# Performance work log

Hardware: AMD Instinct MI355X
Metric: run time of the kernel (lower is better)

## Reference

```python
import jax, jax.numpy as jnp
import numpy as np

NUM_HEADS = 8
NUM_LEVELS = 4
NUM_POINTS = 8
EMBED = 256
SPATIAL_SHAPES = ((92, 160), (46, 80), (23, 40), (12, 20))


def _bilinear_sample(vl, gx, gy, H, W):
    # vl: [N, d, H*W]; gx, gy: [N, Q, P], grid coords in [-1, 1]
    # matches F.grid_sample(mode='bilinear', padding_mode='zeros', align_corners=False)
    x = (gx + 1.0) * (W * 0.5) - 0.5
    y = (gy + 1.0) * (H * 0.5) - 0.5
    x0 = jnp.floor(x)
    y0 = jnp.floor(y)
    wx = x - x0
    wy = y - y0
    x0i = x0.astype(jnp.int32)
    y0i = y0.astype(jnp.int32)
    N, Q, P = gx.shape
    d = vl.shape[1]

    def gather(xi, yi):
        valid = ((xi >= 0) & (xi < W) & (yi >= 0) & (yi < H)).astype(vl.dtype)
        idx = jnp.clip(yi, 0, H - 1) * W + jnp.clip(xi, 0, W - 1)  # [N, Q, P]
        flat = jnp.broadcast_to(idx.reshape(N, 1, Q * P), (N, d, Q * P))
        got = jnp.take_along_axis(vl, flat, axis=2).reshape(N, d, Q, P)
        return got * valid[:, None]

    return (gather(x0i, y0i) * ((1 - wx) * (1 - wy))[:, None]
            + gather(x0i + 1, y0i) * (wx * (1 - wy))[:, None]
            + gather(x0i, y0i + 1) * ((1 - wx) * wy)[:, None]
            + gather(x0i + 1, y0i + 1) * (wx * wy)[:, None])


def _forward(query, value, reference_points, spatial_shapes,
             W_off, b_off, W_attn, b_attn, W_val, b_val, W_out, b_out):
    shapes = np.asarray(spatial_shapes)  # static per-level (H, W)
    bs, Q, C = query.shape
    H, Lv, P = NUM_HEADS, NUM_LEVELS, NUM_POINTS
    d = C // H
    # value projection, split into heads: [bs*H, d, Ltot]
    v = value @ W_val + b_val
    v = v.reshape(bs, -1, H, d).transpose(0, 2, 3, 1).reshape(bs * H, d, -1)
    # sampling offsets [bs, Q, H, Lv, P, 2]
    off = (query @ W_off + b_off).reshape(bs, Q, H, Lv, P, 2)
    # attention weights, softmax over Lv*P
    aw = jax.nn.softmax((query @ W_attn + b_attn).reshape(bs, Q, H, Lv * P), axis=-1)
    aw = aw.reshape(bs, Q, H, Lv, P).transpose(0, 2, 1, 3, 4).reshape(bs * H, Q, Lv, P)
    # normalize offsets by level (W, H)
    norm = jnp.asarray([[w_, h_] for h_, w_ in shapes], dtype=query.dtype)  # [Lv, 2]
    loc = reference_points[:, :, None, :, None, :] + off / norm[None, None, None, :, None, :]
    grids = (2.0 * loc - 1.0).transpose(0, 2, 1, 3, 4, 5).reshape(bs * H, Q, Lv, P, 2)
    out = jnp.zeros((bs * H, d, Q), dtype=query.dtype)
    start = 0
    for lvl in range(Lv):
        H_l, W_l = int(shapes[lvl, 0]), int(shapes[lvl, 1])
        vl = v[:, :, start:start + H_l * W_l]
        g = grids[:, :, lvl]  # [bs*H, Q, P, 2]
        s = _bilinear_sample(vl, g[..., 0], g[..., 1], H_l, W_l)  # [bs*H, d, Q, P]
        out = out + jnp.einsum('ndqp,nqp->ndq', s, aw[:, :, lvl])
        start += H_l * W_l
    out = out.reshape(bs, H, d, Q).transpose(0, 3, 1, 2).reshape(bs, Q, C)
    return out @ W_out + b_out


def setup_inputs() -> dict:
    key = jax.random.key(0)
    ks = jax.random.split(key, 9)
    bs, Q = 6, 4096  # 6 cameras x (64x64 BEV queries)
    Ltot = sum(h * w for h, w in SPATIAL_SHAPES)  # 19560
    HLP2 = NUM_HEADS * NUM_LEVELS * NUM_POINTS * 2  # 512
    HLP = NUM_HEADS * NUM_LEVELS * NUM_POINTS  # 256
    s = 0.02
    return {
        "query": jax.random.normal(ks[0], (bs, Q, EMBED), jnp.float32),
        "value": jax.random.normal(ks[1], (bs, Ltot, EMBED), jnp.float32),
        "reference_points": jax.random.uniform(ks[2], (bs, Q, NUM_LEVELS, 2), jnp.float32),
        "spatial_shapes": jnp.asarray(SPATIAL_SHAPES, jnp.int32),
        "W_off": s * jax.random.normal(ks[3], (EMBED, HLP2), jnp.float32),
        "b_off": s * jax.random.normal(ks[4], (HLP2,), jnp.float32),
        "W_attn": s * jax.random.normal(ks[5], (EMBED, HLP), jnp.float32),
        "b_attn": s * jax.random.normal(ks[6], (HLP,), jnp.float32),
        "W_val": s * jax.random.normal(ks[7], (EMBED, EMBED), jnp.float32),
        "b_val": jnp.zeros((EMBED,), jnp.float32),
        "W_out": s * jax.random.normal(ks[8], (EMBED, EMBED), jnp.float32),
        "b_out": jnp.zeros((EMBED,), jnp.float32),
    }


def reference(query, value, reference_points, spatial_shapes,
              W_off, b_off, W_attn, b_attn, W_val, b_val, W_out, b_out):
    return _forward(query, value, reference_points, spatial_shapes,
                    W_off, b_off, W_attn, b_attn, W_val, b_val, W_out, b_out)
```

## Files before the change

kernel.cpp:

```cpp
#include <hip/hip_runtime.h>
#include <stdint.h>

#define BS 6
#define NQ 4096
#define NH 8
#define EMB 256
#define LTOT 19560
#define ROWS_V 117360
#define ROWS_VP 117376
#define ROWS_Q 24576

typedef __attribute__((ext_vector_type(8))) short bf16x8;
typedef __attribute__((ext_vector_type(4))) float floatx4;
typedef __attribute__((ext_vector_type(8))) unsigned short ushort8v;

__device__ __forceinline__ ushort f2bf(float f) {
    union { float f; uint32_t i; } c; c.f = f;
    uint32_t r = c.i + 0x7FFFu + ((c.i >> 16) & 1u);
    return (ushort)(r >> 16);
}
__device__ __forceinline__ float bflo(uint32_t u) {
    union { uint32_t i; float f; } c; c.i = u << 16; return c.f;
}
__device__ __forceinline__ float bfhi(uint32_t u) {
    union { uint32_t i; float f; } c; c.i = u & 0xFFFF0000u; return c.f;
}

__device__ __forceinline__ void gll16(const ushort* g, ushort* l) {
    __builtin_amdgcn_global_load_lds(
        (const __attribute__((address_space(1))) void*)g,
        (__attribute__((address_space(3))) void*)l, 16, 0, 0);
}

__global__ __launch_bounds__(256) void cast_bf16(
    const float* __restrict__ in, ushort* __restrict__ out, int n)
{
    int i = (blockIdx.x * 256 + threadIdx.x) * 8;
    if (i >= n) return;
    float4 f0 = *(const float4*)(in + i);
    float4 f1 = *(const float4*)(in + i + 4);
    ushort8v r;
    r[0] = f2bf(f0.x); r[1] = f2bf(f0.y); r[2] = f2bf(f0.z); r[3] = f2bf(f0.w);
    r[4] = f2bf(f1.x); r[5] = f2bf(f1.y); r[6] = f2bf(f1.z); r[7] = f2bf(f1.w);
    *(ushort8v*)(out + i) = r;
}

__global__ __launch_bounds__(256) void cast_t(
    const float* __restrict__ W, ushort* __restrict__ Wt, int N_)
{
    int id = blockIdx.x * 256 + threadIdx.x;
    if (id >= 256 * N_) return;
    int n = id >> 8;
    int k = id & 255;
    Wt[id] = f2bf(W[(size_t)k * N_ + n]);
}

__global__ __launch_bounds__(768) void bias_concat(
    const float* __restrict__ b_off, const float* __restrict__ b_attn,
    float* __restrict__ bcat)
{
    int i = threadIdx.x;
    bcat[i] = (i < 512) ? b_off[i] : b_attn[i - 512];
}

__global__ __launch_bounds__(512) void vgemm(
    const float* __restrict__ A,
    const ushort* __restrict__ Bt,
    const float* __restrict__ bias,
    ushort* __restrict__ C)
{
    constexpr int K = 256, N = 256, M = ROWS_V;
    __shared__ ushort As[128 * 32];
    __shared__ ushort Bs[256 * 32];

    const int t = threadIdx.x;
    const int w = t >> 6;
    const int lane = t & 63;
    const int bm = blockIdx.x * 128;
    const int wm = (w >> 2) * 64;
    const int wn = (w & 3) * 64;

    const int arow = t >> 2;
    const int acol = (t & 3) * 8;
    const bool rowok = (bm + arow) < M;
    const float* Ap = A + (size_t)(bm + arow) * K + acol;
    ushort* Asw = &As[arow * 32 + acol];

    const int srow = lane >> 2;
    const int scol = (lane & 3) * 8;
    const ushort* Bg0 = Bt + (size_t)(w * 32 + srow) * K + scol;
    const ushort* Bg1 = Bt + (size_t)(w * 32 + 16 + srow) * K + scol;
    ushort* Bl0 = &Bs[(w * 32) * 32];
    ushort* Bl1 = &Bs[(w * 32 + 16) * 32];

    const ushort* apt = &As[(wm + (lane & 15)) * 32 + (lane >> 4) * 8];
    const ushort* bpt = &Bs[(wn + (lane & 15)) * 32 + (lane >> 4) * 8];

    floatx4 acc[4][4] = {};

    for (int kt = 0; kt < K; kt += 32) {
        float4 f0, f1;
        if (rowok) {
            f0 = *(const float4*)(Ap + kt);
            f1 = *(const float4*)(Ap + kt + 4);
        } else {
            f0 = make_float4(0.f, 0.f, 0.f, 0.f);
            f1 = f0;
        }
        __syncthreads();
        gll16(Bg0 + kt, Bl0);
        gll16(Bg1 + kt, Bl1);
        ushort8v u;
        u[0] = f2bf(f0.x); u[1] = f2bf(f0.y); u[2] = f2bf(f0.z); u[3] = f2bf(f0.w);
        u[4] = f2bf(f1.x); u[5] = f2bf(f1.y); u[6] = f2bf(f1.z); u[7] = f2bf(f1.w);
        *(ushort8v*)Asw = u;
        __syncthreads();

        bf16x8 a[4], b[4];
        #pragma unroll
        for (int i = 0; i < 4; ++i) {
            a[i] = *(const bf16x8*)(apt + i * 16 * 32);
            b[i] = *(const bf16x8*)(bpt + i * 16 * 32);
        }
        #pragma unroll
        for (int i = 0; i < 4; ++i)
            #pragma unroll
            for (int j = 0; j < 4; ++j)
                acc[i][j] = __builtin_amdgcn_mfma_f32_16x16x32_bf16(
                    a[i], b[j], acc[i][j], 0, 0, 0);
    }

    const int crow = (lane >> 4) * 4;
    const int ccol = lane & 15;
    #pragma unroll
    for (int j = 0; j < 4; ++j) {
        int gcol = wn + j * 16 + ccol;
        float bv = bias[gcol];
        #pragma unroll
        for (int i = 0; i < 4; ++i) {
            #pragma unroll
            for (int r = 0; r < 4; ++r) {
                int grow = bm + wm + i * 16 + crow + r;
                if (grow < M)
                    C[(size_t)grow * N + gcol] = f2bf(acc[i][j][r] + bv);
            }
        }
    }
}

__global__ __launch_bounds__(256) void gemm_bt(
    const ushort* __restrict__ A,
    const ushort* __restrict__ Bt,
    const float* __restrict__ bias,
    float* __restrict__ C, int M, int N)
{
    constexpr int K = 256;
    __shared__ ushort As[128 * 32];
    __shared__ ushort Bs[128 * 32];

    const int t = threadIdx.x;
    const int w = t >> 6;
    const int lane = t & 63;
    const int bm = blockIdx.x * 128;
    const int bn = blockIdx.y * 128;
    const int wm = (w >> 1) * 64;
    const int wn = (w & 1) * 64;

    floatx4 acc[4][4] = {};

    const int srow = lane >> 2;
    const int scol = (lane & 3) * 8;
    const ushort* Ag0 = A + (size_t)(bm + (w * 2 + 0) * 16 + srow) * K + scol;
    const ushort* Ag1 = A + (size_t)(bm + (w * 2 + 1) * 16 + srow) * K + scol;
    const ushort* Bg0 = Bt + (size_t)(bn + (w * 2 + 0) * 16 + srow) * K + scol;
    const ushort* Bg1 = Bt + (size_t)(bn + (w * 2 + 1) * 16 + srow) * K + scol;
    ushort* Al0 = &As[(w * 2 + 0) * 512];
    ushort* Al1 = &As[(w * 2 + 1) * 512];
    ushort* Bl0 = &Bs[(w * 2 + 0) * 512];
    ushort* Bl1 = &Bs[(w * 2 + 1) * 512];

    const ushort* apt = &As[(wm + (lane & 15)) * 32 + (lane >> 4) * 8];
    const ushort* bpt = &Bs[(wn + (lane & 15)) * 32 + (lane >> 4) * 8];

    for (int kt = 0; kt < K; kt += 32) {
        __syncthreads();
        gll16(Ag0 + kt, Al0);
        gll16(Ag1 + kt, Al1);
        gll16(Bg0 + kt, Bl0);
        gll16(Bg1 + kt, Bl1);
        __syncthreads();

        bf16x8 a[4], b[4];
        #pragma unroll
        for (int i = 0; i < 4; ++i) {
            a[i] = *(const bf16x8*)(apt + i * 16 * 32);
            b[i] = *(const bf16x8*)(bpt + i * 16 * 32);
        }
        #pragma unroll
        for (int i = 0; i < 4; ++i)
            #pragma unroll
            for (int j = 0; j < 4; ++j)
                acc[i][j] = __builtin_amdgcn_mfma_f32_16x16x32_bf16(
                    a[i], b[j], acc[i][j], 0, 0, 0);
    }

    const int crow = (lane >> 4) * 4;
    const int ccol = lane & 15;
    #pragma unroll
    for (int j = 0; j < 4; ++j) {
        int gcol = bn + wn + j * 16 + ccol;
        float bv = bias[gcol];
        #pragma unroll
        for (int i = 0; i < 4; ++i) {
            #pragma unroll
            for (int r = 0; r < 4; ++r) {
                int grow = bm + wm + i * 16 + crow + r;
                if (grow < M)
                    C[(size_t)grow * N + gcol] = acc[i][j][r] + bv;
            }
        }
    }
}

__global__ __launch_bounds__(256) void sampler4(
    const ushort* __restrict__ v,
    const float* __restrict__ qp,
    const float* __restrict__ ref,
    ushort* __restrict__ agg)
{
    const int tid = threadIdx.x;
    const int g = blockIdx.x * 64 + (tid >> 2);
    const int st = tid & 3;
    const int h = g & 7;
    const int bq = g >> 3;
    const int b = bq >> 12;

    float o[16];
    {
        const float* offp = qp + (size_t)bq * 768 + h * 64 + st * 16;
        #pragma unroll
        for (int i = 0; i < 4; ++i)
            *(float4*)&o[i * 4] = *(const float4*)(offp + i * 4);
    }
    float a8[8];
    {
        const float* lp = qp + (size_t)bq * 768 + 512 + h * 32 + st * 8;
        *(float4*)&a8[0] = *(const float4*)(lp);
        *(float4*)&a8[4] = *(const float4*)(lp + 4);
        float m = a8[0];
        #pragma unroll
        for (int i = 1; i < 8; ++i) m = fmaxf(m, a8[i]);
        m = fmaxf(m, __shfl_xor(m, 1, 4));
        m = fmaxf(m, __shfl_xor(m, 2, 4));
        float s = 0.f;
        #pragma unroll
        for (int i = 0; i < 8; ++i) { a8[i] = __expf(a8[i] - m); s += a8[i]; }
        s += __shfl_xor(s, 1, 4);
        s += __shfl_xor(s, 2, 4);
        float inv = 1.f / s;
        #pragma unroll
        for (int i = 0; i < 8; ++i) a8[i] *= inv;
    }
    float rf[8];
    *(float4*)&rf[0] = *(const float4*)(ref + (size_t)bq * 8);
    *(float4*)&rf[4] = *(const float4*)(ref + (size_t)bq * 8 + 4);

    const ushort* vb = v + (size_t)b * LTOT * EMB + h * 32 + st * 8;

    const int LW[4] = {160, 80, 40, 20};
    const int LH[4] = {92, 46, 23, 12};
    const int LS[4] = {0, 14720, 18400, 19320};

    float acc[8] = {0.f, 0.f, 0.f, 0.f, 0.f, 0.f, 0.f, 0.f};

    #pragma unroll
    for (int k = 0; k < 32; ++k) {
        const int l = k >> 3;
        const int W = LW[l], Hh = LH[l], S = LS[l];
        const int idx = k & 7;
        float awk = __shfl(a8[idx], k >> 3, 4);
        float ox  = __shfl(o[2 * idx], k >> 3, 4);
        float oy  = __shfl(o[2 * idx + 1], k >> 3, 4);

        float px = fmaf(rf[2 * l], (float)W, ox) - 0.5f;
        float py = fmaf(rf[2 * l + 1], (float)Hh, oy) - 0.5f;
        float x0f = floorf(px), y0f = floorf(py);
        float wx = px - x0f, wy = py - y0f;
        int x0 = (int)x0f, y0 = (int)y0f;
        int x1 = x0 + 1, y1 = y0 + 1;

        float vx0 = (x0 >= 0 && x0 < W) ? 1.f : 0.f;
        float vx1 = (x1 >= 0 && x1 < W) ? 1.f : 0.f;
        float vy0 = (y0 >= 0 && y0 < Hh) ? 1.f : 0.f;
        float vy1 = (y1 >= 0 && y1 < Hh) ? 1.f : 0.f;
        int cx0 = min(max(x0, 0), W - 1);
        int cx1 = min(max(x1, 0), W - 1);
        int cy0 = min(max(y0, 0), Hh - 1);
        int cy1 = min(max(y1, 0), Hh - 1);

        float w00 = (1.f - wx) * (1.f - wy) * vx0 * vy0 * awk;
        float w10 = wx * (1.f - wy) * vx1 * vy0 * awk;
        float w01 = (1.f - wx) * wy * vx0 * vy1 * awk;
        float w11 = wx * wy * vx1 * vy1 * awk;

        uint4 c00 = *(const uint4*)(vb + (size_t)(S + cy0 * W + cx0) * EMB);
        uint4 c10 = *(const uint4*)(vb + (size_t)(S + cy0 * W + cx1) * EMB);
        uint4 c01 = *(const uint4*)(vb + (size_t)(S + cy1 * W + cx0) * EMB);
        uint4 c11 = *(const uint4*)(vb + (size_t)(S + cy1 * W + cx1) * EMB);

        #define ACC8(w_, c_) \
            acc[0] = fmaf(w_, bflo(c_.x), acc[0]); acc[1] = fmaf(w_, bfhi(c_.x), acc[1]); \
            acc[2] = fmaf(w_, bflo(c_.y), acc[2]); acc[3] = fmaf(w_, bfhi(c_.y), acc[3]); \
            acc[4] = fmaf(w_, bflo(c_.z), acc[4]); acc[5] = fmaf(w_, bfhi(c_.z), acc[5]); \
            acc[6] = fmaf(w_, bflo(c_.w), acc[6]); acc[7] = fmaf(w_, bfhi(c_.w), acc[7]);
        ACC8(w00, c00);
        ACC8(w10, c10);
        ACC8(w01, c01);
        ACC8(w11, c11);
        #undef ACC8
    }

    ushort8v r;
    #pragma unroll
    for (int i = 0; i < 8; ++i) r[i] = f2bf(acc[i]);
    *(ushort8v*)(agg + (size_t)bq * 256 + h * 32 + st * 8) = r;
}

extern "C" void kernel_launch(void* const* d_in, const int* in_sizes, int n_in,
                              void* d_out, int out_size, void* d_ws, size_t ws_size,
                              hipStream_t stream) {
    const float* query  = (const float*)d_in[0];
    const float* value  = (const float*)d_in[1];
    const float* refpts = (const float*)d_in[2];
    const float* W_off  = (const float*)d_in[4];
    const float* b_off  = (const float*)d_in[5];
    const float* W_attn = (const float*)d_in[6];
    const float* b_attn = (const float*)d_in[7];
    const float* W_val  = (const float*)d_in[8];
    const float* b_val  = (const float*)d_in[9];
    const float* W_out  = (const float*)d_in[10];
    const float* b_out  = (const float*)d_in[11];
    float* out = (float*)d_out;

    char* ws = (char*)d_ws;
    ushort* v_bf   = (ushort*)(ws);
    ushort* q_bf   = (ushort*)(ws + 60096512ull);
    float*  qp     = (float*) (ws + 72679424ull);
    ushort* agg_bf = (ushort*)(ws + 148176896ull);
    ushort* Wvt    = (ushort*)(ws + 160759808ull);
    ushort* Wq     = (ushort*)(ws + 160890880ull);
    ushort* Wot    = (ushort*)(ws + 161284096ull);
    float*  bcat   = (float*) (ws + 161415168ull);

    cast_t<<<(256 * 256) / 256, 256, 0, stream>>>(W_val, Wvt, 256);
    cast_t<<<(256 * 512) / 256, 256, 0, stream>>>(W_off, Wq, 512);
    cast_t<<<(256 * 256) / 256, 256, 0, stream>>>(W_attn, Wq + 512 * 256, 256);
    cast_t<<<(256 * 256) / 256, 256, 0, stream>>>(W_out, Wot, 256);
    bias_concat<<<1, 768, 0, stream>>>(b_off, b_attn, bcat);
    cast_bf16<<<(ROWS_Q * EMB / 8) / 256, 256, 0, stream>>>(
        query, q_bf, ROWS_Q * EMB);

    vgemm<<<ROWS_VP / 128, 512, 0, stream>>>(value, Wvt, b_val, v_bf);

    gemm_bt<<<dim3(ROWS_Q / 128, 6), 256, 0, stream>>>(
        q_bf, Wq, bcat, qp, ROWS_Q, 768);

    sampler4<<<(ROWS_Q * NH) / 64, 256, 0, stream>>>(
        v_bf, qp, refpts, agg_bf);

    gemm_bt<<<dim3(ROWS_Q / 128, 2), 256, 0, stream>>>(
        agg_bf, Wot, b_out, out, ROWS_Q, 256);
}
```

Measured before the change: 416.4 us.

## Keep projected values in fp32, preload full weight tiles, restructure sampler

The value projection now writes fp32 instead of bf16, and the sampler reads fp32 corners. This doubles the value buffer and its gather traffic but drops the bf16 unpacking. The GEMMs preload the whole weight slab into LDS once and stream A directly from global memory into registers, with no per-k-step barriers. The query cast kernel is removed and the query GEMM is fused with that conversion. The sampler gives each lane one level, precomputes corner weights and indices per level, and broadcasts them by shuffle.

```diff
diff --git a/kernel.cpp b/kernel.cpp
--- a/kernel.cpp
+++ b/kernel.cpp
@@ -12,47 +12,61 @@
 
 typedef __attribute__((ext_vector_type(8))) short bf16x8;
 typedef __attribute__((ext_vector_type(4))) float floatx4;
-typedef __attribute__((ext_vector_type(8))) unsigned short ushort8v;
 
 __device__ __forceinline__ ushort f2bf(float f) {
     union { float f; uint32_t i; } c; c.f = f;
     uint32_t r = c.i + 0x7FFFu + ((c.i >> 16) & 1u);
     return (ushort)(r >> 16);
 }
-__device__ __forceinline__ float bflo(uint32_t u) {
-    union { uint32_t i; float f; } c; c.i = u << 16; return c.f;
-}
-__device__ __forceinline__ float bfhi(uint32_t u) {
-    union { uint32_t i; float f; } c; c.i = u & 0xFFFF0000u; return c.f;
-}
-
-__device__ __forceinline__ void gll16(const ushort* g, ushort* l) {
+__device__ __forceinline__ uint32_t pk2bf(float x, float y) {
+    union { float f; uint32_t i; } a, b; a.f = x; b.f = y;
+    return __builtin_amdgcn_perm(b.i + 0x8000u, a.i + 0x8000u, 0x07060302u);
+}
+
+__device__ __forceinline__ void gll16(const void* g, void* l) {
     __builtin_amdgcn_global_load_lds(
         (const __attribute__((address_space(1))) void*)g,
         (__attribute__((address_space(3))) void*)l, 16, 0, 0);
 }
 
-__global__ __launch_bounds__(256) void cast_bf16(
-    const float* __restrict__ in, ushort* __restrict__ out, int n)
-{
-    int i = (blockIdx.x * 256 + threadIdx.x) * 8;
-    if (i >= n) return;
-    float4 f0 = *(const float4*)(in + i);
-    float4 f1 = *(const float4*)(in + i + 4);
-    ushort8v r;
-    r[0] = f2bf(f0.x); r[1] = f2bf(f0.y); r[2] = f2bf(f0.z); r[3] = f2bf(f0.w);
-    r[4] = f2bf(f1.x); r[5] = f2bf(f1.y); r[6] = f2bf(f1.z); r[7] = f2bf(f1.w);
-    *(ushort8v*)(out + i) = r;
-}
-
-__global__ __launch_bounds__(256) void cast_t(
-    const float* __restrict__ W, ushort* __restrict__ Wt, int N_)
+#define PFMA4(d, s, v) \
+    (d).x = fmaf((s), (v).x, (d).x); \
+    (d).y = fmaf((s), (v).y, (d).y); \
+    (d).z = fmaf((s), (v).z, (d).z); \
+    (d).w = fmaf((s), (v).w, (d).w);
+
+__global__ __launch_bounds__(256) void cast_tc(
+    const float* __restrict__ W, ushort* __restrict__ Wt, int N_, int lgNB)
 {
     int id = blockIdx.x * 256 + threadIdx.x;
     if (id >= 256 * N_) return;
-    int n = id >> 8;
-    int k = id & 255;
+    int nb   = id >> (8 + lgNB);
+    int rem  = id & ((256 << lgNB) - 1);
+    int c    = rem >> (5 + lgNB);
+    int rem2 = rem & ((32 << lgNB) - 1);
+    int nl   = rem2 >> 5;
+    int kp   = rem2 & 31;
+    int k = (c << 5) + kp;
+    int n = (nb << lgNB) + nl;
     Wt[id] = f2bf(W[(size_t)k * N_ + n]);
+}
+
+__global__ __launch_bounds__(256) void cast_wq(
+    const float* __restrict__ W_off, const float* __restrict__ W_attn,
+    ushort* __restrict__ Wt)
+{
+    int id = blockIdx.x * 256 + threadIdx.x;
+    int nb   = id >> 16;
+    int rem  = id & 65535;
+    int c    = rem >> 13;
+    int rem2 = rem & 8191;
+    int nl   = rem2 >> 5;
+    int kp   = rem2 & 31;
+    int k = (c << 5) + kp;
+    int n = (nb << 8) + nl;
+    float s = (n < 512) ? W_off[(size_t)k * 512 + n]
+                        : W_attn[(size_t)k * 256 + (n - 512)];
+    Wt[id] = f2bf(s);
 }
 
 __global__ __launch_bounds__(768) void bias_concat(
@@ -63,15 +77,14 @@
     bcat[i] = (i < 512) ? b_off[i] : b_attn[i - 512];
 }
 
-__global__ __launch_bounds__(512) void vgemm(
+__global__ __launch_bounds__(512) void gemm_f32a(
     const float* __restrict__ A,
     const ushort* __restrict__ Bt,
     const float* __restrict__ bias,
-    ushort* __restrict__ C)
-{
-    constexpr int K = 256, N = 256, M = ROWS_V;
-    __shared__ ushort As[128 * 32];
-    __shared__ ushort Bs[256 * 32];
+    float* __restrict__ C,
+    int M, int ldc)
+{
+    __shared__ ushort Bs[256 * 256];
 
     const int t = threadIdx.x;
     const int w = t >> 6;
@@ -80,48 +93,51 @@
     const int wm = (w >> 2) * 64;
     const int wn = (w & 3) * 64;
 
-    const int arow = t >> 2;
-    const int acol = (t & 3) * 8;
-    const bool rowok = (bm + arow) < M;
-    const float* Ap = A + (size_t)(bm + arow) * K + acol;
-    ushort* Asw = &As[arow * 32 + acol];
-
-    const int srow = lane >> 2;
-    const int scol = (lane & 3) * 8;
-    const ushort* Bg0 = Bt + (size_t)(w * 32 + srow) * K + scol;
-    const ushort* Bg1 = Bt + (size_t)(w * 32 + 16 + srow) * K + scol;
-    ushort* Bl0 = &Bs[(w * 32) * 32];
-    ushort* Bl1 = &Bs[(w * 32 + 16) * 32];
-
-    const ushort* apt = &As[(wm + (lane & 15)) * 32 + (lane >> 4) * 8];
-    const ushort* bpt = &Bs[(wn + (lane & 15)) * 32 + (lane >> 4) * 8];
+    {
+        const char* gsrc = (const char*)Bt + t * 16;
+        char* ldst = (char*)Bs + t * 16;
+        #pragma unroll
+        for (int s = 0; s < 16; ++s)
+            gll16(gsrc + s * 8192, ldst + s * 8192);
+    }
+
+    const int ml = lane & 15;
+    const int kq = lane >> 4;
+
+    const float* Ar[4];
+    bool rok[4];
+    #pragma unroll
+    for (int i = 0; i < 4; ++i) {
+        int row = bm + wm + i * 16 + ml;
+        rok[i] = row < M;
+        Ar[i] = A + (size_t)row * 256 + kq * 8;
+    }
 
     floatx4 acc[4][4] = {};
-
-    for (int kt = 0; kt < K; kt += 32) {
-        float4 f0, f1;
-        if (rowok) {
-            f0 = *(const float4*)(Ap + kt);
-            f1 = *(const float4*)(Ap + kt + 4);
-        } else {
-            f0 = make_float4(0.f, 0.f, 0.f, 0.f);
-            f1 = f0;
+    __syncthreads();
+
+    #pragma unroll
+    for (int c = 0; c < 8; ++c) {
+        bf16x8 a[4], b[4];
+        #pragma unroll
+        for (int i = 0; i < 4; ++i) {
+            float4 f0, f1;
+            if (rok[i]) {
+                f0 = *(const float4*)(Ar[i] + c * 32);
+                f1 = *(const float4*)(Ar[i] + c * 32 + 4);
+            } else {
+                f0 = make_float4(0.f, 0.f, 0.f, 0.f); f1 = f0;
+            }
+            union { uint32_t u[4]; bf16x8 v; } pk;
+            pk.u[0] = pk2bf(f0.x, f0.y);
+            pk.u[1] = pk2bf(f0.z, f0.w);
+            pk.u[2] = pk2bf(f1.x, f1.y);
+            pk.u[3] = pk2bf(f1.z, f1.w);
+            a[i] = pk.v;
         }
-        __syncthreads();
-        gll16(Bg0 + kt, Bl0);
-        gll16(Bg1 + kt, Bl1);
-        ushort8v u;
-        u[0] = f2bf(f0.x); u[1] = f2bf(f0.y); u[2] = f2bf(f0.z); u[3] = f2bf(f0.w);
-        u[4] = f2bf(f1.x); u[5] = f2bf(f1.y); u[6] = f2bf(f1.z); u[7] = f2bf(f1.w);
-        *(ushort8v*)Asw = u;
-        __syncthreads();
-
-        bf16x8 a[4], b[4];
-        #pragma unroll
-        for (int i = 0; i < 4; ++i) {
-            a[i] = *(const bf16x8*)(apt + i * 16 * 32);
-            b[i] = *(const bf16x8*)(bpt + i * 16 * 32);
-        }
+        #pragma unroll
+        for (int j = 0; j < 4; ++j)
+            b[j] = *(const bf16x8*)&Bs[(c * 256 + wn + j * 16 + ml) * 32 + kq * 8];
         #pragma unroll
         for (int i = 0; i < 4; ++i)
             #pragma unroll
@@ -142,60 +158,62 @@
             for (int r = 0; r < 4; ++r) {
                 int grow = bm + wm + i * 16 + crow + r;
                 if (grow < M)
-                    C[(size_t)grow * N + gcol] = f2bf(acc[i][j][r] + bv);
+                    C[(size_t)grow * ldc + gcol] = acc[i][j][r] + bv;
             }
         }
     }
 }
 
-__global__ __launch_bounds__(256) void gemm_bt(
+__global__ __launch_bounds__(256) void gemm_bf16a(
     const ushort* __restrict__ A,
     const ushort* __restrict__ Bt,
     const float* __restrict__ bias,
-    float* __restrict__ C, int M, int N)
-{
-    constexpr int K = 256;
-    __shared__ ushort As[128 * 32];
-    __shared__ ushort Bs[128 * 32];
+    float* __restrict__ C,
+    int M, int ldc)
+{
+    __shared__ ushort Bs[128 * 256];
 
     const int t = threadIdx.x;
     const int w = t >> 6;
     const int lane = t & 63;
     const int bm = blockIdx.x * 128;
-    const int bn = blockIdx.y * 128;
     const int wm = (w >> 1) * 64;
     const int wn = (w & 1) * 64;
 
+    {
+        const char* gsrc = (const char*)Bt + t * 16;
+        char* ldst = (char*)Bs + t * 16;
+        #pragma unroll
+        for (int s = 0; s < 16; ++s)
+            gll16(gsrc + s * 4096, ldst + s * 4096);
+    }
+
+    const int ml = lane & 15;
+    const int kq = lane >> 4;
+
+    const ushort* Ar[4];
+    bool rok[4];
+    #pragma unroll
+    for (int i = 0; i < 4; ++i) {
+        int row = bm + wm + i * 16 + ml;
+        rok[i] = row < M;
+        Ar[i] = A + (size_t)row * 256 + kq * 8;
+    }
+
     floatx4 acc[4][4] = {};
-
-    const int srow = lane >> 2;
-    const int scol = (lane & 3) * 8;
-    const ushort* Ag0 = A + (size_t)(bm + (w * 2 + 0) * 16 + srow) * K + scol;
-    const ushort* Ag1 = A + (size_t)(bm + (w * 2 + 1) * 16 + srow) * K + scol;
-    const ushort* Bg0 = Bt + (size_t)(bn + (w * 2 + 0) * 16 + srow) * K + scol;
-    const ushort* Bg1 = Bt + (size_t)(bn + (w * 2 + 1) * 16 + srow) * K + scol;
-    ushort* Al0 = &As[(w * 2 + 0) * 512];
-    ushort* Al1 = &As[(w * 2 + 1) * 512];
-    ushort* Bl0 = &Bs[(w * 2 + 0) * 512];
-    ushort* Bl1 = &Bs[(w * 2 + 1) * 512];
-
-    const ushort* apt = &As[(wm + (lane & 15)) * 32 + (lane >> 4) * 8];
-    const ushort* bpt = &Bs[(wn + (lane & 15)) * 32 + (lane >> 4) * 8];
-
-    for (int kt = 0; kt < K; kt += 32) {
-        __syncthreads();
-        gll16(Ag0 + kt, Al0);
-        gll16(Ag1 + kt, Al1);
-        gll16(Bg0 + kt, Bl0);
-        gll16(Bg1 + kt, Bl1);
-        __syncthreads();
-
+    __syncthreads();
+
+    #pragma unroll
+    for (int c = 0; c < 8; ++c) {
         bf16x8 a[4], b[4];
         #pragma unroll
         for (int i = 0; i < 4; ++i) {
-            a[i] = *(const bf16x8*)(apt + i * 16 * 32);
-            b[i] = *(const bf16x8*)(bpt + i * 16 * 32);
+            if (rok[i]) a[i] = *(const bf16x8*)(Ar[i] + c * 32);
+            else        a[i] = bf16x8{0,0,0,0,0,0,0,0};
         }
+        #pragma unroll
+        for (int j = 0; j < 4; ++j)
+            b[j] = *(const bf16x8*)&Bs[(c * 128 + wn + j * 16 + ml) * 32 + kq * 8];
         #pragma unroll
         for (int i = 0; i < 4; ++i)
             #pragma unroll
@@ -208,7 +226,7 @@
     const int ccol = lane & 15;
     #pragma unroll
     for (int j = 0; j < 4; ++j) {
-        int gcol = bn + wn + j * 16 + ccol;
+        int gcol = wn + j * 16 + ccol;
         float bv = bias[gcol];
         #pragma unroll
         for (int i = 0; i < 4; ++i) {
@@ -216,24 +234,31 @@
             for (int r = 0; r < 4; ++r) {
                 int grow = bm + wm + i * 16 + crow + r;
                 if (grow < M)
-                    C[(size_t)grow * N + gcol] = acc[i][j][r] + bv;
+                    C[(size_t)grow * ldc + gcol] = acc[i][j][r] + bv;
             }
         }
     }
 }
 
-__global__ __launch_bounds__(256) void sampler4(
-    const ushort* __restrict__ v,
+__global__ __launch_bounds__(256) void sampler5(
+    const float* __restrict__ v,
     const float* __restrict__ qp,
     const float* __restrict__ ref,
     ushort* __restrict__ agg)
 {
     const int tid = threadIdx.x;
     const int g = blockIdx.x * 64 + (tid >> 2);
-    const int st = tid & 3;
+    const int st = tid & 2 ? (tid & 1 ? 3 : 2) : (tid & 1 ? 1 : 0);
     const int h = g & 7;
     const int bq = g >> 3;
     const int b = bq >> 12;
+
+    const int W  = (st == 0) ? 160 : (st == 1) ? 80 : (st == 2) ? 40 : 20;
+    const int Hh = (st == 0) ? 92  : (st == 1) ? 46 : (st == 2) ? 23 : 12;
+    const int S  = (st == 0) ? 0 : (st == 1) ? 14720 : (st == 2) ? 18400 : 19320;
+    const float Wf = (float)W, Hf = (float)Hh;
+
+    float2 rf = *(const float2*)(ref + (size_t)bq * 8 + st * 2);
 
     float o[16];
     {
@@ -261,34 +286,17 @@
         #pragma unroll
         for (int i = 0; i < 8; ++i) a8[i] *= inv;
     }
-    float rf[8];
-    *(float4*)&rf[0] = *(const float4*)(ref + (size_t)bq * 8);
-    *(float4*)&rf[4] = *(const float4*)(ref + (size_t)bq * 8 + 4);
-
-    const ushort* vb = v + (size_t)b * LTOT * EMB + h * 32 + st * 8;
-
-    const int LW[4] = {160, 80, 40, 20};
-    const int LH[4] = {92, 46, 23, 12};
-    const int LS[4] = {0, 14720, 18400, 19320};
-
-    float acc[8] = {0.f, 0.f, 0.f, 0.f, 0.f, 0.f, 0.f, 0.f};
-
-    #pragma unroll
-    for (int k = 0; k < 32; ++k) {
-        const int l = k >> 3;
-        const int W = LW[l], Hh = LH[l], S = LS[l];
-        const int idx = k & 7;
-        float awk = __shfl(a8[idx], k >> 3, 4);
-        float ox  = __shfl(o[2 * idx], k >> 3, 4);
-        float oy  = __shfl(o[2 * idx + 1], k >> 3, 4);
-
-        float px = fmaf(rf[2 * l], (float)W, ox) - 0.5f;
-        float py = fmaf(rf[2 * l + 1], (float)Hh, oy) - 0.5f;
+
+    float w00[8], w10[8], w01[8], w11[8];
+    int   i00[8], i10[8], i01[8], i11[8];
+    #pragma unroll
+    for (int j = 0; j < 8; ++j) {
+        float px = fmaf(rf.x, Wf, o[2 * j]) - 0.5f;
+        float py = fmaf(rf.y, Hf, o[2 * j + 1]) - 0.5f;
         float x0f = floorf(px), y0f = floorf(py);
         float wx = px - x0f, wy = py - y0f;
         int x0 = (int)x0f, y0 = (int)y0f;
         int x1 = x0 + 1, y1 = y0 + 1;
-
         float vx0 = (x0 >= 0 && x0 < W) ? 1.f : 0.f;
         float vx1 = (x1 >= 0 && x1 < W) ? 1.f : 0.f;
         float vy0 = (y0 >= 0 && y0 < Hh) ? 1.f : 0.f;
@@ -297,33 +305,56 @@
         int cx1 = min(max(x1, 0), W - 1);
         int cy0 = min(max(y0, 0), Hh - 1);
         int cy1 = min(max(y1, 0), Hh - 1);
-
-        float w00 = (1.f - wx) * (1.f - wy) * vx0 * vy0 * awk;
-        float w10 = wx * (1.f - wy) * vx1 * vy0 * awk;
-        float w01 = (1.f - wx) * wy * vx0 * vy1 * awk;
-        float w11 = wx * wy * vx1 * vy1 * awk;
-
-        uint4 c00 = *(const uint4*)(vb + (size_t)(S + cy0 * W + cx0) * EMB);
-        uint4 c10 = *(const uint4*)(vb + (size_t)(S + cy0 * W + cx1) * EMB);
-        uint4 c01 = *(const uint4*)(vb + (size_t)(S + cy1 * W + cx0) * EMB);
-        uint4 c11 = *(const uint4*)(vb + (size_t)(S + cy1 * W + cx1) * EMB);
-
-        #define ACC8(w_, c_) \
-            acc[0] = fmaf(w_, bflo(c_.x), acc[0]); acc[1] = fmaf(w_, bfhi(c_.x), acc[1]); \
-            acc[2] = fmaf(w_, bflo(c_.y), acc[2]); acc[3] = fmaf(w_, bfhi(c_.y), acc[3]); \
-            acc[4] = fmaf(w_, bflo(c_.z), acc[4]); acc[5] = fmaf(w_, bfhi(c_.z), acc[5]); \
-            acc[6] = fmaf(w_, bflo(c_.w), acc[6]); acc[7] = fmaf(w_, bfhi(c_.w), acc[7]);
-        ACC8(w00, c00);
-        ACC8(w10, c10);
-        ACC8(w01, c01);
-        ACC8(w11, c11);
-        #undef ACC8
-    }
-
-    ushort8v r;
-    #pragma unroll
-    for (int i = 0; i < 8; ++i) r[i] = f2bf(acc[i]);
-    *(ushort8v*)(agg + (size_t)bq * 256 + h * 32 + st * 8) = r;
+        float aj = a8[j];
+        w00[j] = (1.f - wx) * (1.f - wy) * vx0 * vy0 * aj;
+        w10[j] = wx * (1.f - wy) * vx1 * vy0 * aj;
+        w01[j] = (1.f - wx) * wy * vx0 * vy1 * aj;
+        w11[j] = wx * wy * vx1 * vy1 * aj;
+        i00[j] = S + cy0 * W + cx0;
+        i10[j] = S + cy0 * W + cx1;
+        i01[j] = S + cy1 * W + cx0;
+        i11[j] = S + cy1 * W + cx1;
+    }
+
+    const float* vb = v + (size_t)b * LTOT * EMB + h * 32 + st * 8;
+
+    float4 accL = make_float4(0.f, 0.f, 0.f, 0.f);
+    float4 accH = make_float4(0.f, 0.f, 0.f, 0.f);
+
+    #pragma unroll
+    for (int k = 0; k < 32; ++k) {
+        const int own = k >> 3;
+        const int j = k & 7;
+        float W00 = __shfl(w00[j], own, 4);
+        float W10 = __shfl(w10[j], own, 4);
+        float W01 = __shfl(w01[j], own, 4);
+        float W11 = __shfl(w11[j], own, 4);
+        int I00 = __shfl(i00[j], own, 4);
+        int I10 = __shfl(i10[j], own, 4);
+        int I01 = __shfl(i01[j], own, 4);
+        int I11 = __shfl(i11[j], own, 4);
+
+        const float4* p00 = (const float4*)(vb + (size_t)I00 * 256);
+        const float4* p10 = (const float4*)(vb + (size_t)I10 * 256);
+        const float4* p01 = (const float4*)(vb + (size_t)I01 * 256);
+        const float4* p11 = (const float4*)(vb + (size_t)I11 * 256);
+        float4 l00 = p00[0], h00 = p00[1];
+        float4 l10 = p10[0], h10 = p10[1];
+        float4 l01 = p01[0], h01 = p01[1];
+        float4 l11 = p11[0], h11 = p11[1];
+
+        PFMA4(accL, W00, l00); PFMA4(accH, W00, h00);
+        PFMA4(accL, W10, l10); PFMA4(accH, W10, h10);
+        PFMA4(accL, W01, l01); PFMA4(accH, W01, h01);
+        PFMA4(accL, W11, l11); PFMA4(accH, W11, h11);
+    }
+
+    ushort* ap = agg + (size_t)bq * 256 + h * 32 + st * 8;
+    ushort4 r0, r1;
+    r0.x = f2bf(accL.x); r0.y = f2bf(accL.y); r0.z = f2bf(accL.z); r0.w = f2bf(accL.w);
+    r1.x = f2bf(accH.x); r1.y = f2bf(accH.y); r1.z = f2bf(accH.z); r1.w = f2bf(accH.w);
+    *(ushort4*)ap = r0;
+    *(ushort4*)(ap + 4) = r1;
 }
 
 extern "C" void kernel_launch(void* const* d_in, const int* in_sizes, int n_in,
@@ -343,31 +374,32 @@
     float* out = (float*)d_out;
 
     char* ws = (char*)d_ws;
-    ushort* v_bf   = (ushort*)(ws);
-    ushort* q_bf   = (ushort*)(ws + 60096512ull);
-    float*  qp     = (float*) (ws + 72679424ull);
-    ushort* agg_bf = (ushort*)(ws + 148176896ull);
-    ushort* Wvt    = (ushort*)(ws + 160759808ull);
-    ushort* Wq     = (ushort*)(ws + 160890880ull);
-    ushort* Wot    = (ushort*)(ws + 161284096ull);
-    float*  bcat   = (float*) (ws + 161415168ull);
-
-    cast_t<<<(256 * 256) / 256, 256, 0, stream>>>(W_val, Wvt, 256);
-    cast_t<<<(256 * 512) / 256, 256, 0, stream>>>(W_off, Wq, 512);
-    cast_t<<<(256 * 256) / 256, 256, 0, stream>>>(W_attn, Wq + 512 * 256, 256);
-    cast_t<<<(256 * 256) / 256, 256, 0, stream>>>(W_out, Wot, 256);
+    float*  v_f    = (float*) (ws);
+    float*  qp     = (float*) (ws + 120193024ull);
+    ushort* agg_bf = (ushort*)(ws + 195690496ull);
+    ushort* Wvt    = (ushort*)(ws + 208273408ull);
+    ushort* Wq     = (ushort*)(ws + 208404480ull);
+    ushort* Wot    = (ushort*)(ws + 208797696ull);
+    float*  bcat   = (float*) (ws + 208928768ull);
+
+    cast_tc<<<256, 256, 0, stream>>>(W_val, Wvt, 256, 8);
+    cast_wq<<<768, 256, 0, stream>>>(W_off, W_attn, Wq);
+    cast_tc<<<256, 256, 0, stream>>>(W_out, Wot, 256, 7);
     bias_concat<<<1, 768, 0, stream>>>(b_off, b_attn, bcat);
-    cast_bf16<<<(ROWS_Q * EMB / 8) / 256, 256, 0, stream>>>(
-        query, q_bf, ROWS_Q * EMB);
-
-    vgemm<<<ROWS_VP / 128, 512, 0, stream>>>(value, Wvt, b_val, v_bf);
-
-    gemm_bt<<<dim3(ROWS_Q / 128, 6), 256, 0, stream>>>(
-        q_bf, Wq, bcat, qp, ROWS_Q, 768);
-
-    sampler4<<<(ROWS_Q * NH) / 64, 256, 0, stream>>>(
-        v_bf, qp, refpts, agg_bf);
-
-    gemm_bt<<<dim3(ROWS_Q / 128, 2), 256, 0, stream>>>(
-        agg_bf, Wot, b_out, out, ROWS_Q, 256);
-}
+
+    gemm_f32a<<<ROWS_VP / 128, 512, 0, stream>>>(
+        value, Wvt, b_val, v_f, ROWS_V, 256);
+
+    for (int by = 0; by < 3; ++by)
+        gemm_f32a<<<ROWS_Q / 128, 512, 0, stream>>>(
+            query, Wq + (size_t)by * 65536, bcat + by * 256,
+            qp + by * 256, ROWS_Q, 768);
+
+    sampler5<<<(ROWS_Q * NH) / 64, 256, 0, stream>>>(
+        v_f, qp, refpts, agg_bf);
+
+    for (int by = 0; by < 2; ++by)
+        gemm_bf16a<<<ROWS_Q / 128, 256, 0, stream>>>(
+            agg_bf, Wot + (size_t)by * 32768, b_out + by * 128,
+            out + by * 128, ROWS_Q, 256);
+}
```

Measured after the change: 613.0 us. +47.2%, slower.

## Fuse query cast into GEMM, prefetch A tiles, precompute sampler corners per level

Applied to the files above, without the earlier changes.

The separate query cast kernel is dropped, and a templated fp32-input GEMM handles both the value and query projections. The value GEMM moves from one 512-thread block covering all 256 columns to 256-thread blocks covering 128 columns, so the fp32 A rows are read twice. The GEMM now loads the next A k-tile into registers before the MFMAs of the current tile and packs bf16 with a perm-based conversion (round-half-up instead of round-to-nearest-even). In the sampler, each of the four threads per head computes bilinear weights and indices for its own level, and these are shuffled to the others, so coordinate math is no longer repeated per thread.

```diff
diff --git a/kernel.cpp b/kernel.cpp
--- a/kernel.cpp
+++ b/kernel.cpp
@@ -19,6 +19,10 @@
     uint32_t r = c.i + 0x7FFFu + ((c.i >> 16) & 1u);
     return (ushort)(r >> 16);
 }
+__device__ __forceinline__ uint32_t pk2bf(float x, float y) {
+    union { float f; uint32_t i; } a, b; a.f = x; b.f = y;
+    return __builtin_amdgcn_perm(b.i + 0x8000u, a.i + 0x8000u, 0x07060302u);
+}
 __device__ __forceinline__ float bflo(uint32_t u) {
     union { uint32_t i; float f; } c; c.i = u << 16; return c.f;
 }
@@ -26,23 +30,10 @@
     union { uint32_t i; float f; } c; c.i = u & 0xFFFF0000u; return c.f;
 }
 
-__device__ __forceinline__ void gll16(const ushort* g, ushort* l) {
+__device__ __forceinline__ void gll16(const void* g, void* l) {
     __builtin_amdgcn_global_load_lds(
         (const __attribute__((address_space(1))) void*)g,
         (__attribute__((address_space(3))) void*)l, 16, 0, 0);
-}
-
-__global__ __launch_bounds__(256) void cast_bf16(
-    const float* __restrict__ in, ushort* __restrict__ out, int n)
-{
-    int i = (blockIdx.x * 256 + threadIdx.x) * 8;
-    if (i >= n) return;
-    float4 f0 = *(const float4*)(in + i);
-    float4 f1 = *(const float4*)(in + i + 4);
-    ushort8v r;
-    r[0] = f2bf(f0.x); r[1] = f2bf(f0.y); r[2] = f2bf(f0.z); r[3] = f2bf(f0.w);
-    r[4] = f2bf(f1.x); r[5] = f2bf(f1.y); r[6] = f2bf(f1.z); r[7] = f2bf(f1.w);
-    *(ushort8v*)(out + i) = r;
 }
 
 __global__ __launch_bounds__(256) void cast_t(
@@ -63,58 +54,74 @@
     bcat[i] = (i < 512) ? b_off[i] : b_attn[i - 512];
 }
 
-__global__ __launch_bounds__(512) void vgemm(
+template<bool OUT_BF16>
+__global__ __launch_bounds__(256) void gemm_qv(
     const float* __restrict__ A,
     const ushort* __restrict__ Bt,
     const float* __restrict__ bias,
-    ushort* __restrict__ C)
-{
-    constexpr int K = 256, N = 256, M = ROWS_V;
+    void* __restrict__ Cv,
+    int M, int ldc)
+{
+    constexpr int K = 256;
     __shared__ ushort As[128 * 32];
-    __shared__ ushort Bs[256 * 32];
+    __shared__ ushort Bs[128 * 32];
 
     const int t = threadIdx.x;
     const int w = t >> 6;
     const int lane = t & 63;
     const int bm = blockIdx.x * 128;
-    const int wm = (w >> 2) * 64;
-    const int wn = (w & 3) * 64;
-
-    const int arow = t >> 2;
-    const int acol = (t & 3) * 8;
+    const int bn = blockIdx.y * 128;
+    const int wm = (w >> 1) * 64;
+    const int wn = (w & 1) * 64;
+
+    const int srow = lane >> 2;
+    const int scol = (lane & 3) * 8;
+    const ushort* Bg0 = Bt + (size_t)(bn + w * 32 + srow) * K + scol;
+    const ushort* Bg1 = Bt + (size_t)(bn + w * 32 + 16 + srow) * K + scol;
+    ushort* Bl0 = &Bs[(w * 32) * 32];
+    ushort* Bl1 = &Bs[(w * 32 + 16) * 32];
+
+    const int arow = t >> 1;
+    const int acol = (t & 1) * 16;
     const bool rowok = (bm + arow) < M;
     const float* Ap = A + (size_t)(bm + arow) * K + acol;
     ushort* Asw = &As[arow * 32 + acol];
 
-    const int srow = lane >> 2;
-    const int scol = (lane & 3) * 8;
-    const ushort* Bg0 = Bt + (size_t)(w * 32 + srow) * K + scol;
-    const ushort* Bg1 = Bt + (size_t)(w * 32 + 16 + srow) * K + scol;
-    ushort* Bl0 = &Bs[(w * 32) * 32];
-    ushort* Bl1 = &Bs[(w * 32 + 16) * 32];
-
     const ushort* apt = &As[(wm + (lane & 15)) * 32 + (lane >> 4) * 8];
     const ushort* bpt = &Bs[(wn + (lane & 15)) * 32 + (lane >> 4) * 8];
 
     floatx4 acc[4][4] = {};
 
+    float4 c0, c1, c2, c3;
+    if (rowok) {
+        c0 = *(const float4*)(Ap);
+        c1 = *(const float4*)(Ap + 4);
+        c2 = *(const float4*)(Ap + 8);
+        c3 = *(const float4*)(Ap + 12);
+    } else {
+        c0 = make_float4(0.f, 0.f, 0.f, 0.f);
+        c1 = c0; c2 = c0; c3 = c0;
+    }
+
     for (int kt = 0; kt < K; kt += 32) {
-        float4 f0, f1;
-        if (rowok) {
-            f0 = *(const float4*)(Ap + kt);
-            f1 = *(const float4*)(Ap + kt + 4);
-        } else {
-            f0 = make_float4(0.f, 0.f, 0.f, 0.f);
-            f1 = f0;
-        }
         __syncthreads();
         gll16(Bg0 + kt, Bl0);
         gll16(Bg1 + kt, Bl1);
-        ushort8v u;
-        u[0] = f2bf(f0.x); u[1] = f2bf(f0.y); u[2] = f2bf(f0.z); u[3] = f2bf(f0.w);
-        u[4] = f2bf(f1.x); u[5] = f2bf(f1.y); u[6] = f2bf(f1.z); u[7] = f2bf(f1.w);
-        *(ushort8v*)Asw = u;
+        uint4 u0, u1;
+        u0.x = pk2bf(c0.x, c0.y); u0.y = pk2bf(c0.z, c0.w);
+        u0.z = pk2bf(c1.x, c1.y); u0.w = pk2bf(c1.z, c1.w);
+        u1.x = pk2bf(c2.x, c2.y); u1.y = pk2bf(c2.z, c2.w);
+        u1.z = pk2bf(c3.x, c3.y); u1.w = pk2bf(c3.z, c3.w);
+        *(uint4*)Asw = u0;
+        *(uint4*)(Asw + 8) = u1;
         __syncthreads();
+
+        if (kt + 32 < K && rowok) {
+            c0 = *(const float4*)(Ap + kt + 32);
+            c1 = *(const float4*)(Ap + kt + 36);
+            c2 = *(const float4*)(Ap + kt + 40);
+            c3 = *(const float4*)(Ap + kt + 44);
+        }
 
         bf16x8 a[4], b[4];
         #pragma unroll
@@ -134,15 +141,20 @@
     const int ccol = lane & 15;
     #pragma unroll
     for (int j = 0; j < 4; ++j) {
-        int gcol = wn + j * 16 + ccol;
+        int gcol = bn + wn + j * 16 + ccol;
         float bv = bias[gcol];
         #pragma unroll
         for (int i = 0; i < 4; ++i) {
             #pragma unroll
             for (int r = 0; r < 4; ++r) {
                 int grow = bm + wm + i * 16 + crow + r;
-                if (grow < M)
-                    C[(size_t)grow * N + gcol] = f2bf(acc[i][j][r] + bv);
+                if (grow < M) {
+                    float val = acc[i][j][r] + bv;
+                    if (OUT_BF16)
+                        ((ushort*)Cv)[(size_t)grow * ldc + gcol] = f2bf(val);
+                    else
+                        ((float*)Cv)[(size_t)grow * ldc + gcol] = val;
+                }
             }
         }
     }
@@ -222,7 +234,7 @@
     }
 }
 
-__global__ __launch_bounds__(256) void sampler4(
+__global__ __launch_bounds__(256) void sampler6(
     const ushort* __restrict__ v,
     const float* __restrict__ qp,
     const float* __restrict__ ref,
@@ -235,6 +247,13 @@
     const int bq = g >> 3;
     const int b = bq >> 12;
 
+    const int W  = (st == 0) ? 160 : (st == 1) ? 80 : (st == 2) ? 40 : 20;
+    const int Hh = (st == 0) ? 92  : (st == 1) ? 46 : (st == 2) ? 23 : 12;
+    const int S  = (st == 0) ? 0 : (st == 1) ? 14720 : (st == 2) ? 18400 : 19320;
+    const float Wf = (float)W, Hf = (float)Hh;
+
+    float2 rf = *(const float2*)(ref + (size_t)bq * 8 + st * 2);
+
     float o[16];
     {
         const float* offp = qp + (size_t)bq * 768 + h * 64 + st * 16;
@@ -261,34 +280,17 @@
         #pragma unroll
         for (int i = 0; i < 8; ++i) a8[i] *= inv;
     }
-    float rf[8];
-    *(float4*)&rf[0] = *(const float4*)(ref + (size_t)bq * 8);
-    *(float4*)&rf[4] = *(const float4*)(ref + (size_t)bq * 8 + 4);
-
-    const ushort* vb = v + (size_t)b * LTOT * EMB + h * 32 + st * 8;
-
-    const int LW[4] = {160, 80, 40, 20};
-    const int LH[4] = {92, 46, 23, 12};
-    const int LS[4] = {0, 14720, 18400, 19320};
-
-    float acc[8] = {0.f, 0.f, 0.f, 0.f, 0.f, 0.f, 0.f, 0.f};
-
-    #pragma unroll
-    for (int k = 0; k < 32; ++k) {
-        const int l = k >> 3;
-        const int W = LW[l], Hh = LH[l], S = LS[l];
-        const int idx = k & 7;
-        float awk = __shfl(a8[idx], k >> 3, 4);
-        float ox  = __shfl(o[2 * idx], k >> 3, 4);
-        float oy  = __shfl(o[2 * idx + 1], k >> 3, 4);
-
-        float px = fmaf(rf[2 * l], (float)W, ox) - 0.5f;
-        float py = fmaf(rf[2 * l + 1], (float)Hh, oy) - 0.5f;
+
+    float w00[8], w10[8], w01[8], w11[8];
+    int   i00[8], i10[8], i01[8], i11[8];
+    #pragma unroll
+    for (int j = 0; j < 8; ++j) {
+        float px = fmaf(rf.x, Wf, o[2 * j]) - 0.5f;
+        float py = fmaf(rf.y, Hf, o[2 * j + 1]) - 0.5f;
         float x0f = floorf(px), y0f = floorf(py);
         float wx = px - x0f, wy = py - y0f;
         int x0 = (int)x0f, y0 = (int)y0f;
         int x1 = x0 + 1, y1 = y0 + 1;
-
         float vx0 = (x0 >= 0 && x0 < W) ? 1.f : 0.f;
         float vx1 = (x1 >= 0 && x1 < W) ? 1.f : 0.f;
         float vy0 = (y0 >= 0 && y0 < Hh) ? 1.f : 0.f;
@@ -297,26 +299,48 @@
         int cx1 = min(max(x1, 0), W - 1);
         int cy0 = min(max(y0, 0), Hh - 1);
         int cy1 = min(max(y1, 0), Hh - 1);
-
-        float w00 = (1.f - wx) * (1.f - wy) * vx0 * vy0 * awk;
-        float w10 = wx * (1.f - wy) * vx1 * vy0 * awk;
-        float w01 = (1.f - wx) * wy * vx0 * vy1 * awk;
-        float w11 = wx * wy * vx1 * vy1 * awk;
-
-        uint4 c00 = *(const uint4*)(vb + (size_t)(S + cy0 * W + cx0) * EMB);
-        uint4 c10 = *(const uint4*)(vb + (size_t)(S + cy0 * W + cx1) * EMB);
-        uint4 c01 = *(const uint4*)(vb + (size_t)(S + cy1 * W + cx0) * EMB);
-        uint4 c11 = *(const uint4*)(vb + (size_t)(S + cy1 * W + cx1) * EMB);
+        float aj = a8[j];
+        w00[j] = (1.f - wx) * (1.f - wy) * vx0 * vy0 * aj;
+        w10[j] = wx * (1.f - wy) * vx1 * vy0 * aj;
+        w01[j] = (1.f - wx) * wy * vx0 * vy1 * aj;
+        w11[j] = wx * wy * vx1 * vy1 * aj;
+        i00[j] = S + cy0 * W + cx0;
+        i10[j] = S + cy0 * W + cx1;
+        i01[j] = S + cy1 * W + cx0;
+        i11[j] = S + cy1 * W + cx1;
+    }
+
+    const ushort* vb = v + (size_t)b * LTOT * EMB + h * 32 + st * 8;
+
+    float acc[8] = {0.f, 0.f, 0.f, 0.f, 0.f, 0.f, 0.f, 0.f};
+
+    #pragma unroll
+    for (int k = 0; k < 32; ++k) {
+        const int own = k >> 3;
+        const int j = k & 7;
+        float W00 = __shfl(w00[j], own, 4);
+        float W10 = __shfl(w10[j], own, 4);
+        float W01 = __shfl(w01[j], own, 4);
+        float W11 = __shfl(w11[j], own, 4);
+        int I00 = __shfl(i00[j], own, 4);
+        int I10 = __shfl(i10[j], own, 4);
+        int I01 = __shfl(i01[j], own, 4);
+        int I11 = __shfl(i11[j], own, 4);
+
+        uint4 c00 = *(const uint4*)(vb + (size_t)I00 * EMB);
+        uint4 c10 = *(const uint4*)(vb + (size_t)I10 * EMB);
+        uint4 c01 = *(const uint4*)(vb + (size_t)I01 * EMB);
+        uint4 c11 = *(const uint4*)(vb + (size_t)I11 * EMB);
 
         #define ACC8(w_, c_) \
             acc[0] = fmaf(w_, bflo(c_.x), acc[0]); acc[1] = fmaf(w_, bfhi(c_.x), acc[1]); \
             acc[2] = fmaf(w_, bflo(c_.y), acc[2]); acc[3] = fmaf(w_, bfhi(c_.y), acc[3]); \
             acc[4] = fmaf(w_, bflo(c_.z), acc[4]); acc[5] = fmaf(w_, bfhi(c_.z), acc[5]); \
             acc[6] = fmaf(w_, bflo(c_.w), acc[6]); acc[7] = fmaf(w_, bfhi(c_.w), acc[7]);
-        ACC8(w00, c00);
-        ACC8(w10, c10);
-        ACC8(w01, c01);
-        ACC8(w11, c11);
+        ACC8(W00, c00);
+        ACC8(W10, c10);
+        ACC8(W01, c01);
+        ACC8(W11, c11);
         #undef ACC8
     }
 
@@ -344,28 +368,26 @@
 
     char* ws = (char*)d_ws;
     ushort* v_bf   = (ushort*)(ws);
-    ushort* q_bf   = (ushort*)(ws + 60096512ull);
-    float*  qp     = (float*) (ws + 72679424ull);
-    ushort* agg_bf = (ushort*)(ws + 148176896ull);
-    ushort* Wvt    = (ushort*)(ws + 160759808ull);
-    ushort* Wq     = (ushort*)(ws + 160890880ull);
-    ushort* Wot    = (ushort*)(ws + 161284096ull);
-    float*  bcat   = (float*) (ws + 161415168ull);
-
-    cast_t<<<(256 * 256) / 256, 256, 0, stream>>>(W_val, Wvt, 256);
-    cast_t<<<(256 * 512) / 256, 256, 0, stream>>>(W_off, Wq, 512);
-    cast_t<<<(256 * 256) / 256, 256, 0, stream>>>(W_attn, Wq + 512 * 256, 256);
-    cast_t<<<(256 * 256) / 256, 256, 0, stream>>>(W_out, Wot, 256);
+    float*  qp     = (float*) (ws + 60096512ull);
+    ushort* agg_bf = (ushort*)(ws + 135593984ull);
+    ushort* Wvt    = (ushort*)(ws + 148176896ull);
+    ushort* Wq     = (ushort*)(ws + 148307968ull);
+    ushort* Wot    = (ushort*)(ws + 148701184ull);
+    float*  bcat   = (float*) (ws + 148832256ull);
+
+    cast_t<<<256, 256, 0, stream>>>(W_val, Wvt, 256);
+    cast_t<<<512, 256, 0, stream>>>(W_off, Wq, 512);
+    cast_t<<<256, 256, 0, stream>>>(W_attn, Wq + 512 * 256, 256);
+    cast_t<<<256, 256, 0, stream>>>(W_out, Wot, 256);
     bias_concat<<<1, 768, 0, stream>>>(b_off, b_attn, bcat);
-    cast_bf16<<<(ROWS_Q * EMB / 8) / 256, 256, 0, stream>>>(
-        query, q_bf, ROWS_Q * EMB);
-
-    vgemm<<<ROWS_VP / 128, 512, 0, stream>>>(value, Wvt, b_val, v_bf);
-
-    gemm_bt<<<dim3(ROWS_Q / 128, 6), 256, 0, stream>>>(
-        q_bf, Wq, bcat, qp, ROWS_Q, 768);
-
-    sampler4<<<(ROWS_Q * NH) / 64, 256, 0, stream>>>(
+
+    gemm_qv<true><<<dim3(ROWS_VP / 128, 2), 256, 0, stream>>>(
+        value, Wvt, b_val, v_bf, ROWS_V, 256);
+
+    gemm_qv<false><<<dim3(ROWS_Q / 128, 6), 256, 0, stream>>>(
+        query, Wq, bcat, qp, ROWS_Q, 768);
+
+    sampler6<<<(ROWS_Q * NH) / 64, 256, 0, stream>>>(
         v_bf, qp, refpts, agg_bf);
 
     gemm_bt<<<dim3(ROWS_Q / 128, 2), 256, 0, stream>>>(
```

After: 434.2 us. +4.3%, slower.
